# Performance work log

Measured on AMD Instinct MI355X. Metric: run time of the kernel, lower is better.

## Reference

```python
import jax, jax.numpy as jnp
import numpy as np

B, T, E = 2, 2048, 1024   # batch, block_size, emb_d
H, D = 16, 64             # heads, head_size


def setup_inputs() -> dict:
    key = jax.random.key(0)
    ks = jax.random.split(key, 7)
    s = 1.0 / np.sqrt(E)
    inputs = jax.random.normal(ks[0], (B, T, E), dtype=jnp.float32)
    k_w = jax.random.uniform(ks[1], (H, E, D), jnp.float32, -s, s)
    k_b = jax.random.uniform(ks[2], (H, D), jnp.float32, -s, s)
    q_w = jax.random.uniform(ks[3], (H, E, D), jnp.float32, -s, s)
    q_b = jax.random.uniform(ks[4], (H, D), jnp.float32, -s, s)
    v_w = jax.random.uniform(ks[5], (H, E, D), jnp.float32, -s, s)
    v_b = jax.random.uniform(ks[6], (H, D), jnp.float32, -s, s)
    return {"inputs": inputs, "k_w": k_w, "k_b": k_b,
            "q_w": q_w, "q_b": q_b, "v_w": v_w, "v_b": v_b}


def reference(inputs, k_w, k_b, q_w, q_b, v_w, v_b):
    # Per-head linear projections, vectorized over heads: (B,T,E)x(H,E,D)->(B,H,T,D)
    k = jnp.einsum('bte,hed->bhtd', inputs, k_w) + k_b[None, :, None, :]
    q = jnp.einsum('bte,hed->bhtd', inputs, q_w) + q_b[None, :, None, :]
    v = jnp.einsum('bte,hed->bhtd', inputs, v_w) + v_b[None, :, None, :]

    scale = D ** (-0.5)
    # scores: (B,H,Tq,Tk)
    w = jnp.einsum('bhtd,bhsd->bhts', q, k) * scale
    tril = jnp.tril(jnp.ones((T, T), dtype=bool))
    w = jnp.where(tril[None, None, :, :], w, -jnp.inf)
    # NOTE: original torch code does softmax(weights, dim=1) on a (B,T,T)
    # tensor, i.e. over the QUERY axis. Faithfully reproduce: axis=-2 here.
    w = jax.nn.softmax(w, axis=-2)
    out = jnp.einsum('bhts,bhsd->bhtd', w, v)           # (B,H,T,D)
    # concat heads along last dim, head-major order matching torch.cat
    return out.transpose(0, 2, 1, 3).reshape(B, T, H * D)
```

## Files before the change

kernel.cpp:

```cpp
#include <hip/hip_runtime.h>
#include <hip/hip_bf16.h>
#include <math.h>

#define B_ 2
#define T_ 2048
#define E_ 1024
#define H_ 16
#define D_ 64
#define NT_ 32
#define QSCALE 0.180336880f

typedef __attribute__((ext_vector_type(8))) short bf16x8;
typedef __attribute__((ext_vector_type(4))) float f32x4;

#if __has_builtin(__builtin_amdgcn_exp2f)
#define EXP2(x) __builtin_amdgcn_exp2f(x)
#else
#define EXP2(x) exp2f(x)
#endif

__device__ __forceinline__ unsigned short f2bf(float x) {
  union { float f; unsigned u; } v; v.f = x;
  unsigned r = v.u + 0x7FFFu + ((v.u >> 16) & 1u);
  return (unsigned short)(r >> 16);
}
__device__ __forceinline__ unsigned pk2bf(float a, float b) {
  __hip_bfloat162 h = __float22bfloat162_rn(make_float2(a, b));
  union { __hip_bfloat162 h; unsigned u; } c; c.h = h; return c.u;
}

__device__ __forceinline__ void dma8(const unsigned short* g, int gstride,
                                     unsigned short* l, int lane)
{
  const int r = lane >> 3, bg = (lane & 7) ^ (r & 7);
  __builtin_amdgcn_global_load_lds(
      (const __attribute__((address_space(1))) void*)(g + (size_t)r * gstride + bg * 8),
      (__attribute__((address_space(3))) void*)l, 16, 0, 0);
}
__device__ __forceinline__ bf16x8 frag(const unsigned short* tile, int row, int g) {
  return *(const bf16x8*)(tile + row * 64 + (((g ^ row) & 7) << 3));
}

__global__ __launch_bounds__(256) void pack_kernel(
    const float* __restrict__ in, unsigned short* __restrict__ o16,
    const float* __restrict__ qw, const float* __restrict__ kw, const float* __restrict__ vw,
    unsigned short* __restrict__ qwt, unsigned short* __restrict__ kwt,
    unsigned short* __restrict__ vwt)
{
  __shared__ float s[64][65];
  const int tid = threadIdx.x;
  if (blockIdx.x < 2048) {
    const size_t i = ((size_t)blockIdx.x * 256 + tid) * 8;
    float4 f0 = *(const float4*)(in + i);
    float4 f1 = *(const float4*)(in + i + 4);
    unsigned u[4] = { pk2bf(f0.x, f0.y), pk2bf(f0.z, f0.w),
                      pk2bf(f1.x, f1.y), pk2bf(f1.z, f1.w) };
    *(bf16x8*)(o16 + i) = *(const bf16x8*)u;
    return;
  }
  const int i = blockIdx.x - 2048;
  const int e0 = (i & 15) * 64, h = (i >> 4) & 15, z = i >> 8;
  const float* w = (z == 0) ? qw : (z == 1) ? kw : vw;
  unsigned short* o = (z == 0) ? qwt : (z == 1) ? kwt : vwt;
  {
    const int r = tid >> 2;
    #pragma unroll
    for (int p = 0; p < 4; ++p) {
      const int c = (tid & 3) * 4 + p * 16;
      float4 f = *(const float4*)(w + ((size_t)(h * E_ + e0 + r)) * D_ + c);
      s[r][c] = f.x; s[r][c+1] = f.y; s[r][c+2] = f.z; s[r][c+3] = f.w;
    }
  }
  __syncthreads();
  {
    const int d = tid >> 2, ec = (tid & 3) * 16;
    unsigned short tmp[16];
    #pragma unroll
    for (int j = 0; j < 16; ++j) tmp[j] = f2bf(s[ec + j][d]);
    unsigned short* dst = o + ((size_t)(h * D_ + d)) * E_ + e0 + ec;
    *(bf16x8*)(dst)     = *(const bf16x8*)&tmp[0];
    *(bf16x8*)(dst + 8) = *(const bf16x8*)&tmp[8];
  }
}

__global__ __launch_bounds__(256) void proj_kernel(
    const unsigned short* __restrict__ in16,
    const unsigned short* __restrict__ qwt, const unsigned short* __restrict__ kwt,
    const unsigned short* __restrict__ vwt,
    const float* __restrict__ qb, const float* __restrict__ kb, const float* __restrict__ vb,
    unsigned short* __restrict__ qo, unsigned short* __restrict__ ko,
    unsigned short* __restrict__ vt)
{
  __shared__ __align__(16) unsigned short in_s[2][128 * 64];
  __shared__ __align__(16) unsigned short w_s[2][3 * 64 * 64];
  const int tid = threadIdx.x;
  const int lane = tid & 63, wv = tid >> 6;
  const int l15 = lane & 15, quad = lane >> 4;
  const int t0 = blockIdx.x * 128, h = blockIdx.y, b = blockIdx.z;
  const int bh = b * H_ + h;
  const unsigned short* wts[3] = { qwt, kwt, vwt };

  f32x4 acc[3][8];
  #pragma unroll
  for (int x = 0; x < 3; ++x)
    #pragma unroll
    for (int tb = 0; tb < 8; ++tb) acc[x][tb] = (f32x4){0.f, 0.f, 0.f, 0.f};

#define PROJ_STAGE(e0_, bi_)                                                      \
  {                                                                               \
    const unsigned short* gin = in16 + ((size_t)(b * T_ + t0)) * E_ + (e0_);      \
    _Pragma("unroll")                                                             \
    for (int p = 0; p < 4; ++p) {                                                 \
      const int br = wv * 32 + p * 8;                                             \
      dma8(gin + (size_t)br * E_, E_, &in_s[bi_][br * 64], lane);                 \
    }                                                                             \
    _Pragma("unroll")                                                             \
    for (int j = 0; j < 6; ++j) {                                                 \
      const int idx = wv * 6 + j;                                                 \
      const int x = idx >> 3, br = (idx & 7) * 8;                                 \
      dma8(wts[x] + ((size_t)(h * D_ + br)) * E_ + (e0_), E_,                     \
           &w_s[bi_][x * 4096 + br * 64], lane);                                  \
    }                                                                             \
  }

  PROJ_STAGE(0, 0);
  __syncthreads();
  for (int e = 0; e < 16; ++e) {
    const int bi = e & 1;
    if (e < 15) PROJ_STAGE((e + 1) * 64, bi ^ 1);
    const unsigned short* is = in_s[bi];
    const unsigned short* ws = w_s[bi];
    #pragma unroll
    for (int kk = 0; kk < 2; ++kk) {
      const int g0 = kk * 4 + quad;
      bf16x8 bfr[3];
      #pragma unroll
      for (int x = 0; x < 3; ++x)
        bfr[x] = frag(ws, x * 64 + wv * 16 + l15, g0);
      bf16x8 afr[8];
      #pragma unroll
      for (int tb = 0; tb < 8; ++tb)
        afr[tb] = frag(is, tb * 16 + l15, g0);
      #pragma unroll
      for (int tb = 0; tb < 8; ++tb) {
        acc[0][tb] = __builtin_amdgcn_mfma_f32_16x16x32_bf16(bfr[0], afr[tb], acc[0][tb], 0, 0, 0);
        acc[1][tb] = __builtin_amdgcn_mfma_f32_16x16x32_bf16(bfr[1], afr[tb], acc[1][tb], 0, 0, 0);
        acc[2][tb] = __builtin_amdgcn_mfma_f32_16x16x32_bf16(afr[tb], bfr[2], acc[2][tb], 0, 0, 0);
      }
    }
    __syncthreads();
  }
#undef PROJ_STAGE

  const size_t obase = (size_t)bh * T_;
  #pragma unroll
  for (int x = 0; x < 2; ++x) {
    const float scl = (x == 0) ? QSCALE : 1.0f;
    const float* bias = (x == 0) ? qb : kb;
    unsigned short* outp = (x == 0) ? qo : ko;
    float bias4[4];
    *(float4*)bias4 = *(const float4*)&bias[h * D_ + wv * 16 + quad * 4];
    #pragma unroll
    for (int tb = 0; tb < 8; ++tb) {
      const int t = t0 + tb * 16 + l15;
      unsigned short pk[4];
      #pragma unroll
      for (int r = 0; r < 4; ++r) pk[r] = f2bf((acc[x][tb][r] + bias4[r]) * scl);
      *(ushort4*)(outp + (obase + t) * D_ + wv * 16 + quad * 4) = *(const ushort4*)pk;
    }
  }
  {
    const int d = wv * 16 + l15;
    const float bvv = vb[h * D_ + d];
    #pragma unroll
    for (int tb = 0; tb < 8; ++tb) {
      const int t = t0 + tb * 16 + quad * 4;
      unsigned short pk[4];
      #pragma unroll
      for (int r = 0; r < 4; ++r) pk[r] = f2bf(acc[2][tb][r] + bvv);
      *(ushort4*)(vt + ((size_t)(bh * D_ + d)) * T_ + t) = *(const ushort4*)pk;
    }
  }
}

__global__ __launch_bounds__(256) void stats_kernel(
    const unsigned short* __restrict__ q, const unsigned short* __restrict__ k,
    float* __restrict__ lg)
{
  __shared__ __align__(16) unsigned short q_s[2][64 * 64];
  __shared__ float red[4][64];
  const int tid = threadIdx.x;
  const int lane = tid & 63, wv = tid >> 6;
  const int l15 = lane & 15, quad = lane >> 4;
  const int h = blockIdx.x, b = blockIdx.y, sa = blockIdx.z;
  const int bh = b * H_ + h;
  const int s0 = sa * 64;
  const unsigned short* qbase = q + (size_t)bh * T_ * 64;

  bf16x8 kf[4][2];
  #pragma unroll
  for (int nb = 0; nb < 4; ++nb)
    #pragma unroll
    for (int kk = 0; kk < 2; ++kk)
      kf[nb][kk] = *(const bf16x8*)(k + ((size_t)(bh * T_ + s0 + nb * 16 + l15)) * 64
                                      + kk * 32 + quad * 8);

  #pragma unroll
  for (int pp = 0; pp < 2; ++pp) {
    const int br = wv * 16 + pp * 8;
    dma8(qbase + (size_t)(sa * 64 + br) * 64, 64, &q_s[0][br * 64], lane);
  }
  __syncthreads();

  float lsum[4] = {0.f, 0.f, 0.f, 0.f};

  for (int tt = sa, i = 0; tt < NT_; ++tt, ++i) {
    const int bi = i & 1;
    if (tt + 1 < NT_) {
      #pragma unroll
      for (int pp = 0; pp < 2; ++pp) {
        const int br = wv * 16 + pp * 8;
        dma8(qbase + (size_t)((tt + 1) * 64 + br) * 64, 64, &q_s[bi ^ 1][br * 64], lane);
      }
    }
    bf16x8 a0 = frag(q_s[bi], wv * 16 + l15, quad);
    bf16x8 a1 = frag(q_s[bi], wv * 16 + l15, 4 + quad);
    f32x4 sacc[4];
    #pragma unroll
    for (int nb = 0; nb < 4; ++nb) sacc[nb] = (f32x4){0.f, 0.f, 0.f, 0.f};
    #pragma unroll
    for (int nb = 0; nb < 4; ++nb) {
      sacc[nb] = __builtin_amdgcn_mfma_f32_16x16x32_bf16(a0, kf[nb][0], sacc[nb], 0, 0, 0);
      sacc[nb] = __builtin_amdgcn_mfma_f32_16x16x32_bf16(a1, kf[nb][1], sacc[nb], 0, 0, 0);
    }
    if (tt == sa) {
      const int tbase = tt * 64 + wv * 16 + quad * 4;
      #pragma unroll
      for (int nb = 0; nb < 4; ++nb) {
        const int s = s0 + nb * 16 + l15;
        #pragma unroll
        for (int r = 0; r < 4; ++r)
          lsum[nb] += (tbase + r >= s) ? EXP2(sacc[nb][r]) : 0.f;
      }
    } else {
      #pragma unroll
      for (int nb = 0; nb < 4; ++nb)
        #pragma unroll
        for (int r = 0; r < 4; ++r) lsum[nb] += EXP2(sacc[nb][r]);
    }
    __syncthreads();
  }
  #pragma unroll
  for (int nb = 0; nb < 4; ++nb) {
    lsum[nb] += __shfl_xor(lsum[nb], 16);
    lsum[nb] += __shfl_xor(lsum[nb], 32);
  }
  if (lane < 16) {
    #pragma unroll
    for (int nb = 0; nb < 4; ++nb) red[wv][nb * 16 + lane] = lsum[nb];
  }
  __syncthreads();
  if (tid < 64) {
    const float L = red[0][tid] + red[1][tid] + red[2][tid] + red[3][tid];
    lg[(size_t)bh * T_ + s0 + tid] = -__log2f(L);
  }
}

__global__ __launch_bounds__(256) void out_kernel(
    const unsigned short* __restrict__ q, const unsigned short* __restrict__ k,
    const unsigned short* __restrict__ vt, const float* __restrict__ lg,
    float* __restrict__ out)
{
  __shared__ __align__(16) unsigned short k_s[2][64 * 64];
  __shared__ __align__(16) unsigned short vt_s[2][64 * 64];
  __shared__ __align__(16) unsigned short u_s[4][16][72];
  __shared__ float lg_sh[2][64];
  const int tid = threadIdx.x;
  const int lane = tid & 63, wv = tid >> 6;
  const int l15 = lane & 15, quad = lane >> 4;
  const int h = blockIdx.x, b = blockIdx.y, jt = 31 - blockIdx.z;
  const int bh = b * H_ + h;
  const int t0 = jt * 64;
  const unsigned short* kbase = k + (size_t)bh * T_ * 64;
  const unsigned short* vbase = vt + (size_t)bh * D_ * T_;
  const float* lgbase = lg + (size_t)bh * T_;

  const unsigned short* qrow = q + (size_t)(bh * T_ + t0 + wv * 16 + l15) * 64;
  bf16x8 qf0 = *(const bf16x8*)(qrow + quad * 8);
  bf16x8 qf1 = *(const bf16x8*)(qrow + 32 + quad * 8);

  #pragma unroll
  for (int pp = 0; pp < 2; ++pp) {
    const int br = wv * 16 + pp * 8;
    dma8(kbase + (size_t)br * 64, 64, &k_s[0][br * 64], lane);
    dma8(vbase + (size_t)br * T_, T_, &vt_s[0][br * 64], lane);
  }
  if (tid < 64) lg_sh[0][tid] = lgbase[tid];
  __syncthreads();

  f32x4 oacc[4];
  #pragma unroll
  for (int nb = 0; nb < 4; ++nb) oacc[nb] = (f32x4){0.f, 0.f, 0.f, 0.f};

  unsigned short* urow = &u_s[wv][l15][0];
  const int tcol = t0 + wv * 16 + l15;

  for (int st = 0; st <= jt; ++st) {
    const int bi = st & 1;
    if (st < jt) {
      const int s1 = (st + 1) * 64;
      #pragma unroll
      for (int pp = 0; pp < 2; ++pp) {
        const int br = wv * 16 + pp * 8;
        dma8(kbase + (size_t)(s1 + br) * 64, 64, &k_s[bi ^ 1][br * 64], lane);
        dma8(vbase + (size_t)br * T_ + s1, T_, &vt_s[bi ^ 1][br * 64], lane);
      }
      if (tid < 64) lg_sh[bi ^ 1][tid] = lgbase[s1 + tid];
    }
    const int s0 = st * 64;
    const unsigned short* ks = k_s[bi];
    const unsigned short* vs = vt_s[bi];
    const float* lgb = lg_sh[bi];
    f32x4 sacc[4];
    #pragma unroll
    for (int mb = 0; mb < 4; ++mb) {
      float lg4[4];
      *(float4*)lg4 = *(const float4*)&lgb[mb * 16 + quad * 4];
      sacc[mb] = (f32x4){lg4[0], lg4[1], lg4[2], lg4[3]};
    }
    #pragma unroll
    for (int mb = 0; mb < 4; ++mb) {
      bf16x8 ka0 = frag(ks, mb * 16 + l15, quad);
      bf16x8 ka1 = frag(ks, mb * 16 + l15, 4 + quad);
      sacc[mb] = __builtin_amdgcn_mfma_f32_16x16x32_bf16(ka0, qf0, sacc[mb], 0, 0, 0);
      sacc[mb] = __builtin_amdgcn_mfma_f32_16x16x32_bf16(ka1, qf1, sacc[mb], 0, 0, 0);
    }
    if (st == jt) {
      #pragma unroll
      for (int mb = 0; mb < 4; ++mb) {
        const int sbase = s0 + mb * 16 + quad * 4;
        float uu[4] = { EXP2(sacc[mb][0]), EXP2(sacc[mb][1]),
                        EXP2(sacc[mb][2]), EXP2(sacc[mb][3]) };
        #pragma unroll
        for (int r = 0; r < 4; ++r) if (tcol < sbase + r) uu[r] = 0.f;
        *(uint2*)(urow + mb * 16 + quad * 4) =
            make_uint2(pk2bf(uu[0], uu[1]), pk2bf(uu[2], uu[3]));
      }
    } else {
      #pragma unroll
      for (int mb = 0; mb < 4; ++mb) {
        float uu[4] = { EXP2(sacc[mb][0]), EXP2(sacc[mb][1]),
                        EXP2(sacc[mb][2]), EXP2(sacc[mb][3]) };
        *(uint2*)(urow + mb * 16 + quad * 4) =
            make_uint2(pk2bf(uu[0], uu[1]), pk2bf(uu[2], uu[3]));
      }
    }
    #pragma unroll
    for (int kk = 0; kk < 2; ++kk) {
      bf16x8 ua = *(const bf16x8*)(urow + kk * 32 + quad * 8);
      #pragma unroll
      for (int nb = 0; nb < 4; ++nb)
        oacc[nb] = __builtin_amdgcn_mfma_f32_16x16x32_bf16(
            frag(vs, nb * 16 + l15, kk * 4 + quad), ua, oacc[nb], 0, 0, 0);
    }
    __syncthreads();
  }
  float* orow = out + ((size_t)(b * T_ + t0 + wv * 16 + l15)) * (H_ * D_) + h * D_;
  #pragma unroll
  for (int nb = 0; nb < 4; ++nb) {
    float o4[4] = { oacc[nb][0], oacc[nb][1], oacc[nb][2], oacc[nb][3] };
    *(float4*)(orow + nb * 16 + quad * 4) = *(const float4*)o4;
  }
}

extern "C" void kernel_launch(void* const* d_in, const int* in_sizes, int n_in,
                              void* d_out, int out_size, void* d_ws, size_t ws_size,
                              hipStream_t stream) {
  const float* in = (const float*)d_in[0];
  const float* kw = (const float*)d_in[1];
  const float* kb = (const float*)d_in[2];
  const float* qw = (const float*)d_in[3];
  const float* qb = (const float*)d_in[4];
  const float* vw = (const float*)d_in[5];
  const float* vb = (const float*)d_in[6];
  float* out = (float*)d_out;

  unsigned short* p = (unsigned short*)d_ws;
  const size_t inz = (size_t)B_ * T_ * E_;
  const size_t wz  = (size_t)H_ * D_ * E_;
  const size_t qz  = (size_t)B_ * H_ * T_ * D_;
  unsigned short* in16 = p;            p += inz;
  unsigned short* qwt  = p;            p += wz;
  unsigned short* kwt  = p;            p += wz;
  unsigned short* vwt  = p;            p += wz;
  unsigned short* q16  = p;            p += qz;
  unsigned short* k16  = p;            p += qz;
  unsigned short* vtb  = p;            p += qz;
  float* lgbuf = (float*)p;

  dim3 blk(256);
  pack_kernel <<<dim3(2048 + 768), blk, 0, stream>>>(in, in16, qw, kw, vw, qwt, kwt, vwt);
  proj_kernel <<<dim3(T_ / 128, H_, B_), blk, 0, stream>>>(in16, qwt, kwt, vwt,
                                                           qb, kb, vb, q16, k16, vtb);
  stats_kernel<<<dim3(H_, B_, NT_), blk, 0, stream>>>(q16, k16, lgbuf);
  out_kernel  <<<dim3(H_, B_, NT_), blk, 0, stream>>>(q16, k16, vtb, lgbuf, out);
}
```

Baseline: 171.2 us.

## Split out_kernel waves over 2x2 query/key sub-tiles with cross-wave reduction

The four waves of out_kernel now form a 2x2 grid: each wave covers 32 query rows and 32 key columns of the 64x64 tile instead of 16 query rows over all 64 keys. Each K fragment load is reused across two query sub-tiles, and on the diagonal step the fully masked sub-tile is skipped. Partial output accumulators from the two key-halves are combined through shared memory at the end. The cost is more accumulator registers (8 f32x4 instead of 4), an extra LDS reduction with a barrier, and a wave that sits idle on the diagonal step.

```diff
diff --git a/kernel.cpp b/kernel.cpp
--- a/kernel.cpp
+++ b/kernel.cpp
@@ -273,11 +273,12 @@
 {
   __shared__ __align__(16) unsigned short k_s[2][64 * 64];
   __shared__ __align__(16) unsigned short vt_s[2][64 * 64];
-  __shared__ __align__(16) unsigned short u_s[4][16][72];
+  __shared__ __align__(16) unsigned short u_s[4][32][40];
   __shared__ float lg_sh[2][64];
   const int tid = threadIdx.x;
   const int lane = tid & 63, wv = tid >> 6;
   const int l15 = lane & 15, quad = lane >> 4;
+  const int th = wv >> 1, sh = wv & 1;
   const int h = blockIdx.x, b = blockIdx.y, jt = 31 - blockIdx.z;
   const int bh = b * H_ + h;
   const int t0 = jt * 64;
@@ -285,9 +286,13 @@
   const unsigned short* vbase = vt + (size_t)bh * D_ * T_;
   const float* lgbase = lg + (size_t)bh * T_;
 
-  const unsigned short* qrow = q + (size_t)(bh * T_ + t0 + wv * 16 + l15) * 64;
-  bf16x8 qf0 = *(const bf16x8*)(qrow + quad * 8);
-  bf16x8 qf1 = *(const bf16x8*)(qrow + 32 + quad * 8);
+  bf16x8 qf[2][2];
+  #pragma unroll
+  for (int nt = 0; nt < 2; ++nt) {
+    const unsigned short* qrow = q + (size_t)(bh * T_ + t0 + th * 32 + nt * 16 + l15) * 64;
+    qf[nt][0] = *(const bf16x8*)(qrow + quad * 8);
+    qf[nt][1] = *(const bf16x8*)(qrow + 32 + quad * 8);
+  }
 
   #pragma unroll
   for (int pp = 0; pp < 2; ++pp) {
@@ -298,12 +303,11 @@
   if (tid < 64) lg_sh[0][tid] = lgbase[tid];
   __syncthreads();
 
-  f32x4 oacc[4];
-  #pragma unroll
-  for (int nb = 0; nb < 4; ++nb) oacc[nb] = (f32x4){0.f, 0.f, 0.f, 0.f};
-
-  unsigned short* urow = &u_s[wv][l15][0];
-  const int tcol = t0 + wv * 16 + l15;
+  f32x4 oacc[4][2];
+  #pragma unroll
+  for (int mb = 0; mb < 4; ++mb)
+    #pragma unroll
+    for (int nt = 0; nt < 2; ++nt) oacc[mb][nt] = (f32x4){0.f, 0.f, 0.f, 0.f};
 
   for (int st = 0; st <= jt; ++st) {
     const int bi = st & 1;
@@ -317,59 +321,81 @@
       }
       if (tid < 64) lg_sh[bi ^ 1][tid] = lgbase[s1 + tid];
     }
-    const int s0 = st * 64;
     const unsigned short* ks = k_s[bi];
     const unsigned short* vs = vt_s[bi];
     const float* lgb = lg_sh[bi];
-    f32x4 sacc[4];
-    #pragma unroll
-    for (int mb = 0; mb < 4; ++mb) {
-      float lg4[4];
-      *(float4*)lg4 = *(const float4*)&lgb[mb * 16 + quad * 4];
-      sacc[mb] = (f32x4){lg4[0], lg4[1], lg4[2], lg4[3]};
-    }
-    #pragma unroll
-    for (int mb = 0; mb < 4; ++mb) {
-      bf16x8 ka0 = frag(ks, mb * 16 + l15, quad);
-      bf16x8 ka1 = frag(ks, mb * 16 + l15, 4 + quad);
-      sacc[mb] = __builtin_amdgcn_mfma_f32_16x16x32_bf16(ka0, qf0, sacc[mb], 0, 0, 0);
-      sacc[mb] = __builtin_amdgcn_mfma_f32_16x16x32_bf16(ka1, qf1, sacc[mb], 0, 0, 0);
-    }
-    if (st == jt) {
+
+    const bool dead = (st == jt) && (th == 0) && (sh == 1);
+    if (!dead) {
+      f32x4 sacc[2][2];
+      #pragma unroll
+      for (int mb = 0; mb < 2; ++mb) {
+        float lg4[4];
+        *(float4*)lg4 = *(const float4*)&lgb[sh * 32 + mb * 16 + quad * 4];
+        #pragma unroll
+        for (int nt = 0; nt < 2; ++nt)
+          sacc[mb][nt] = (f32x4){lg4[0], lg4[1], lg4[2], lg4[3]};
+      }
+      #pragma unroll
+      for (int mb = 0; mb < 2; ++mb) {
+        bf16x8 ka0 = frag(ks, sh * 32 + mb * 16 + l15, quad);
+        bf16x8 ka1 = frag(ks, sh * 32 + mb * 16 + l15, 4 + quad);
+        #pragma unroll
+        for (int nt = 0; nt < 2; ++nt) {
+          sacc[mb][nt] = __builtin_amdgcn_mfma_f32_16x16x32_bf16(ka0, qf[nt][0], sacc[mb][nt], 0, 0, 0);
+          sacc[mb][nt] = __builtin_amdgcn_mfma_f32_16x16x32_bf16(ka1, qf[nt][1], sacc[mb][nt], 0, 0, 0);
+        }
+      }
+      const bool diagmask = (st == jt) && (th == sh);
+      #pragma unroll
+      for (int mb = 0; mb < 2; ++mb)
+        #pragma unroll
+        for (int nt = 0; nt < 2; ++nt) {
+          float uu[4] = { EXP2(sacc[mb][nt][0]), EXP2(sacc[mb][nt][1]),
+                          EXP2(sacc[mb][nt][2]), EXP2(sacc[mb][nt][3]) };
+          if (diagmask) {
+            const int tl = nt * 16 + l15, sl = mb * 16 + quad * 4;
+            #pragma unroll
+            for (int r = 0; r < 4; ++r) if (tl < sl + r) uu[r] = 0.f;
+          }
+          *(uint2*)(&u_s[wv][nt * 16 + l15][mb * 16 + quad * 4]) =
+              make_uint2(pk2bf(uu[0], uu[1]), pk2bf(uu[2], uu[3]));
+        }
+      #pragma unroll
+      for (int nt = 0; nt < 2; ++nt) {
+        bf16x8 ua = *(const bf16x8*)(&u_s[wv][nt * 16 + l15][quad * 8]);
+        #pragma unroll
+        for (int mb = 0; mb < 4; ++mb)
+          oacc[mb][nt] = __builtin_amdgcn_mfma_f32_16x16x32_bf16(
+              frag(vs, mb * 16 + l15, sh * 4 + quad), ua, oacc[mb][nt], 0, 0, 0);
+      }
+    }
+    __syncthreads();
+  }
+
+  float* scr = (float*)k_s;
+  if (sh == 1) {
+    #pragma unroll
+    for (int mb = 0; mb < 4; ++mb)
+      #pragma unroll
+      for (int nt = 0; nt < 2; ++nt) {
+        float o4[4] = { oacc[mb][nt][0], oacc[mb][nt][1], oacc[mb][nt][2], oacc[mb][nt][3] };
+        *(float4*)&scr[((th * 8 + mb * 2 + nt) * 64 + lane) * 4] = *(const float4*)o4;
+      }
+  }
+  __syncthreads();
+  if (sh == 0) {
+    #pragma unroll
+    for (int nt = 0; nt < 2; ++nt) {
+      float* orow = out + ((size_t)(b * T_ + t0 + th * 32 + nt * 16 + l15)) * (H_ * D_) + h * D_;
       #pragma unroll
       for (int mb = 0; mb < 4; ++mb) {
-        const int sbase = s0 + mb * 16 + quad * 4;
-        float uu[4] = { EXP2(sacc[mb][0]), EXP2(sacc[mb][1]),
-                        EXP2(sacc[mb][2]), EXP2(sacc[mb][3]) };
-        #pragma unroll
-        for (int r = 0; r < 4; ++r) if (tcol < sbase + r) uu[r] = 0.f;
-        *(uint2*)(urow + mb * 16 + quad * 4) =
-            make_uint2(pk2bf(uu[0], uu[1]), pk2bf(uu[2], uu[3]));
-      }
-    } else {
-      #pragma unroll
-      for (int mb = 0; mb < 4; ++mb) {
-        float uu[4] = { EXP2(sacc[mb][0]), EXP2(sacc[mb][1]),
-                        EXP2(sacc[mb][2]), EXP2(sacc[mb][3]) };
-        *(uint2*)(urow + mb * 16 + quad * 4) =
-            make_uint2(pk2bf(uu[0], uu[1]), pk2bf(uu[2], uu[3]));
-      }
-    }
-    #pragma unroll
-    for (int kk = 0; kk < 2; ++kk) {
-      bf16x8 ua = *(const bf16x8*)(urow + kk * 32 + quad * 8);
-      #pragma unroll
-      for (int nb = 0; nb < 4; ++nb)
-        oacc[nb] = __builtin_amdgcn_mfma_f32_16x16x32_bf16(
-            frag(vs, nb * 16 + l15, kk * 4 + quad), ua, oacc[nb], 0, 0, 0);
-    }
-    __syncthreads();
-  }
-  float* orow = out + ((size_t)(b * T_ + t0 + wv * 16 + l15)) * (H_ * D_) + h * D_;
-  #pragma unroll
-  for (int nb = 0; nb < 4; ++nb) {
-    float o4[4] = { oacc[nb][0], oacc[nb][1], oacc[nb][2], oacc[nb][3] };
-    *(float4*)(orow + nb * 16 + quad * 4) = *(const float4*)o4;
+        float4 p = *(const float4*)&scr[((th * 8 + mb * 2 + nt) * 64 + lane) * 4];
+        float o4[4] = { oacc[mb][nt][0] + p.x, oacc[mb][nt][1] + p.y,
+                        oacc[mb][nt][2] + p.z, oacc[mb][nt][3] + p.w };
+        *(float4*)(orow + mb * 16 + quad * 4) = *(const float4*)o4;
+      }
+    }
   }
 }
 
```

Result: no change. 169.9 us (-0.8%).
